# Kernel optimization log

Hardware: AMD Instinct MI355X
Metric: run time of the kernel (lower is better)

## Reference

```python
import jax, jax.numpy as jnp
import numpy as np

# LIF constants from __init__ defaults and forward body
TAU = 20.0        # membrane time constant
TH = 1.0          # base threshold
TAU_ADAPT = 100.0 # adaptation time constant
BETA_ADAPT = 1.5  # adaptation strength
V_RESET = -0.5    # reset potential
K = 10.0          # surrogate sigmoid slope


def setup_inputs() -> dict:
    key = jax.random.key(0)
    I = jax.random.normal(key, (16384, 2048), dtype=jnp.float32)
    return {"I": I}


def reference(I):
    # I: (B, L). Sequential LIF recurrence over L via lax.scan.
    B, L = I.shape
    dtype = I.dtype

    def step(carry, I_t):
        v, a, s_num = carry  # each (B,)
        th_eff = TH + BETA_ADAPT * a
        v = v - v / TAU + I_t  # v += dv
        s_soft = jax.nn.sigmoid(K * (v - th_eff))
        s_hard = (v >= th_eff).astype(dtype)
        # straight-through: forward value = s_hard, grad flows via s_soft
        s = jax.lax.stop_gradient(s_hard - s_soft) + s_soft
        s_num = s_num + s
        s_det = jax.lax.stop_gradient(s)  # reset is non-differentiable (detached)
        v = v * (1.0 - s_det) + V_RESET * s_det
        a = a - a / TAU_ADAPT + s
        return (v, a, s_num), (s, s_num)

    zeros = jnp.zeros((B,), dtype)
    _, (spikes_t, series_t) = jax.lax.scan(step, (zeros, zeros, zeros), I.T)
    # scan outputs are (L, B); transpose back to (B, L)
    return spikes_t.T, series_t.T
```

## Files before the change

### kernel.cpp

```cpp
#include <hip/hip_runtime.h>


#define LIF_L  2048
#define TILE   64
#define NTILES (LIF_L / TILE)

typedef float f32x2 __attribute__((ext_vector_type(2)));

constexpr float kR20 = -0.5f / 20.0f;
constexpr float kC0  = -0.5f - kR20;

__device__ __forceinline__ float lif_step(float Inext, f32x2& x, float& th,
                                          float& carry) {
    const f32x2 C1 = {0.05f, 0.01f};
    const f32x2 C2 = {-20.0f, -100.0f};
    const f32x2 M1 = {-1.0f, -1.0f};
    bool fire = (x.x >= th);
    float s = fire ? 1.0f : 0.0f;
    f32x2 q   = x * C1;
    f32x2 r   = __builtin_elementwise_fma(C2, q, x);
    f32x2 d   = __builtin_elementwise_fma(r, C1, q);
    f32x2 dec = __builtin_elementwise_fma(d, M1, x);
    dec.x = fire ? kC0 : dec.x;
    f32x2 t = {Inext, s};
    x = dec + t;
    carry = __fadd_rn(carry, s);
    th = __fadd_rn(1.0f, __fmul_rn(1.5f, x.y));
    return s;
}

__global__ __launch_bounds__(64, 1) void lif_fwd(const float* __restrict__ I,
                                                 float* __restrict__ spikes,
                                                 float* __restrict__ series) {
    const int lane = threadIdx.x;
    const int row  = blockIdx.x * 64 + lane;

    const float4* __restrict__ I4 =
        reinterpret_cast<const float4*>(I + (size_t)row * LIF_L);
    float4* __restrict__ sp4 =
        reinterpret_cast<float4*>(spikes + (size_t)row * LIF_L);
    float4* __restrict__ se4 =
        reinterpret_cast<float4*>(series + (size_t)row * LIF_L);

    f32x2 x = {0.0f, 0.0f};
    float th = 1.0f, carry = 0.0f;
    float4 bufA[16], bufB[16];

    #pragma unroll
    for (int i = 0; i < 16; ++i) bufA[i] = I4[i];
    #pragma unroll
    for (int i = 0; i < 16; ++i) bufB[i] = I4[16 + i];

    auto compute_tile = [&](const float4* buf, float nx0, int kt) {
        #pragma unroll
        for (int c = 0; c < 16; ++c) {
            float4 in = buf[c];
            float nxt = (c < 15) ? buf[c + 1].x : nx0;
            float4 os, oc;
            os.x = lif_step(in.y, x, th, carry); oc.x = carry;
            os.y = lif_step(in.z, x, th, carry); oc.y = carry;
            os.z = lif_step(in.w, x, th, carry); oc.z = carry;
            os.w = lif_step(nxt,  x, th, carry); oc.w = carry;
            sp4[kt * 16 + c] = os;
            se4[kt * 16 + c] = oc;
        }
    };

    x.x = bufA[0].x;

    for (int p = 0; p < NTILES / 2; ++p) {
        const int kt = 2 * p;
        compute_tile(bufA, bufB[0].x, kt);
        if (kt + 2 < NTILES) {
            #pragma unroll
            for (int i = 0; i < 16; ++i) bufA[i] = I4[(kt + 2) * 16 + i];
        }
        float nx0 = (kt + 2 < NTILES) ? bufA[0].x : 0.0f;
        compute_tile(bufB, nx0, kt + 1);
        if (kt + 3 < NTILES) {
            #pragma unroll
            for (int i = 0; i < 16; ++i) bufB[i] = I4[(kt + 3) * 16 + i];
        }
    }
}

extern "C" void kernel_launch(void* const* d_in, const int* in_sizes, int n_in,
                              void* d_out, int out_size, void* d_ws, size_t ws_size,
                              hipStream_t stream) {
    const float* I = (const float*)d_in[0];
    const int B = in_sizes[0] / LIF_L;
    float* spikes = (float*)d_out;
    float* series = (float*)d_out + (size_t)B * LIF_L;

    const int threads = 64;
    const int blocks = B / 64;
    lif_fwd<<<blocks, threads, 0, stream>>>(I, spikes, series);
}
```

Baseline: 407.4 us.

## Stage output tiles through swizzled LDS for coalesced global stores

Each thread's spike and series outputs now go into a double-buffered, XOR-swizzled shared-memory tile instead of straight to global memory. The previous tile is flushed while the next one is computed, so a wave writes 16 consecutive float4 per row and the stores become coalesced rather than strided by a full row per lane. This relies on a single-wave block, since no barrier separates the LDS writes from the reads. It adds LDS traffic and 64KB of shared memory per block, which may limit occupancy.

```diff
diff --git a/kernel.cpp b/kernel.cpp
--- a/kernel.cpp
+++ b/kernel.cpp
@@ -29,18 +29,21 @@
     return s;
 }
 
+__device__ __forceinline__ int sw_idx(int row, int g) {
+    return row * 64 + (((g) ^ (row & 15)) << 2);
+}
+
 __global__ __launch_bounds__(64, 1) void lif_fwd(const float* __restrict__ I,
                                                  float* __restrict__ spikes,
                                                  float* __restrict__ series) {
+    __shared__ float sp_tile[2][64 * 64];
+    __shared__ float se_tile[2][64 * 64];
+
     const int lane = threadIdx.x;
-    const int row  = blockIdx.x * 64 + lane;
+    const int row0 = blockIdx.x * 64;
 
     const float4* __restrict__ I4 =
-        reinterpret_cast<const float4*>(I + (size_t)row * LIF_L);
-    float4* __restrict__ sp4 =
-        reinterpret_cast<float4*>(spikes + (size_t)row * LIF_L);
-    float4* __restrict__ se4 =
-        reinterpret_cast<float4*>(series + (size_t)row * LIF_L);
+        reinterpret_cast<const float4*>(I + (size_t)(row0 + lane) * LIF_L);
 
     f32x2 x = {0.0f, 0.0f};
     float th = 1.0f, carry = 0.0f;
@@ -51,7 +54,23 @@
     #pragma unroll
     for (int i = 0; i < 16; ++i) bufB[i] = I4[16 + i];
 
-    auto compute_tile = [&](const float4* buf, float nx0, int kt) {
+    auto flush_unit = [&](int i, int tkt, const float* psp, const float* pse) {
+        int row = i * 4 + (lane >> 4);
+        int g   = lane & 15;
+        int ix  = sw_idx(row, g);
+        float4 vs = *reinterpret_cast<const float4*>(&psp[ix]);
+        float4 ve = *reinterpret_cast<const float4*>(&pse[ix]);
+        size_t gaddr = (size_t)(row0 + row) * LIF_L + (size_t)tkt * TILE
+                       + (size_t)g * 4;
+        *reinterpret_cast<float4*>(spikes + gaddr) = vs;
+        *reinterpret_cast<float4*>(series + gaddr) = ve;
+    };
+
+    auto tile = [&](const float4* buf, float nx0, int kt) {
+        float* sp = sp_tile[kt & 1];
+        float* se = se_tile[kt & 1];
+        const float* psp = sp_tile[(kt & 1) ^ 1];
+        const float* pse = se_tile[(kt & 1) ^ 1];
         #pragma unroll
         for (int c = 0; c < 16; ++c) {
             float4 in = buf[c];
@@ -61,8 +80,9 @@
             os.y = lif_step(in.z, x, th, carry); oc.y = carry;
             os.z = lif_step(in.w, x, th, carry); oc.z = carry;
             os.w = lif_step(nxt,  x, th, carry); oc.w = carry;
-            sp4[kt * 16 + c] = os;
-            se4[kt * 16 + c] = oc;
+            *reinterpret_cast<float4*>(&sp[sw_idx(lane, c)]) = os;
+            *reinterpret_cast<float4*>(&se[sw_idx(lane, c)]) = oc;
+            if (kt > 0) flush_unit(c, kt - 1, psp, pse);
         }
     };
 
@@ -70,17 +90,21 @@
 
     for (int p = 0; p < NTILES / 2; ++p) {
         const int kt = 2 * p;
-        compute_tile(bufA, bufB[0].x, kt);
+        tile(bufA, bufB[0].x, kt);
         if (kt + 2 < NTILES) {
             #pragma unroll
             for (int i = 0; i < 16; ++i) bufA[i] = I4[(kt + 2) * 16 + i];
         }
         float nx0 = (kt + 2 < NTILES) ? bufA[0].x : 0.0f;
-        compute_tile(bufB, nx0, kt + 1);
+        tile(bufB, nx0, kt + 1);
         if (kt + 3 < NTILES) {
             #pragma unroll
             for (int i = 0; i < 16; ++i) bufB[i] = I4[(kt + 3) * 16 + i];
         }
+    }
+    #pragma unroll
+    for (int i = 0; i < 16; ++i) {
+        flush_unit(i, NTILES - 1, sp_tile[1], se_tile[1]);
     }
 }
 
```

New measurement: 381.9 us. -6.2%, faster.
